# Kernel tuning notes

Hardware: AMD Instinct MI355X
Metric: run time of the kernel (lower is better)

## Reference

```python
import jax, jax.numpy as jnp
import numpy as np

GROUP_MANTISSA = 8
GROUP_SIZE = 36


def bfp_quantize(x, mantissa=GROUP_MANTISSA, group_size=GROUP_SIZE):
    """Block floating point: flatten, group consecutive group_size elements,
    share the max exponent within each group, keep `mantissa` mantissa bits."""
    flat = x.reshape(-1)
    n = flat.shape[0]
    pad = (-n) % group_size
    f = jnp.pad(flat, (0, pad)).reshape(-1, group_size)  # [G, group_size]
    m = jnp.max(jnp.abs(f), axis=1, keepdims=True)       # group max magnitude
    safe_m = jnp.where(m > 0, m, jnp.ones_like(m))
    e = jnp.floor(jnp.log2(safe_m))                      # shared exponent
    scale = jnp.exp2(e - (mantissa - 1))                 # LSB step for the group
    q = jnp.round(f / scale) * scale
    q = jnp.where(m > 0, q, jnp.zeros_like(q))
    return q.reshape(-1)[:n].reshape(x.shape)


def setup_inputs() -> dict:
    key = jax.random.key(0)
    kx, kw, kb = jax.random.split(key, 3)
    x = jax.random.normal(kx, (32, 64, 112, 112), dtype=jnp.float32)
    # kaiming-uniform-ish scale for a 3x3x64 fan-in
    fan_in = 64 * 3 * 3
    bound = 1.0 / np.sqrt(fan_in)
    weight = jax.random.uniform(kw, (64, 64, 3, 3), dtype=jnp.float32, minval=-bound, maxval=bound) * np.sqrt(3.0)
    bias = jax.random.uniform(kb, (64,), dtype=jnp.float32, minval=-bound, maxval=bound)
    return {"x": x, "weight": weight, "bias": bias}


def reference(x, weight, bias):
    xq = bfp_quantize(x)
    wq = bfp_quantize(weight)
    out = jax.lax.conv_general_dilated(
        xq, wq,
        window_strides=(1, 1),
        padding=((1, 1), (1, 1)),
        lhs_dilation=(1, 1),
        rhs_dilation=(1, 1),
        dimension_numbers=("NCHW", "OIHW", "NCHW"),
        feature_group_count=1,
    )
    return out + bias[None, :, None, None]
```

## Files before the change

kernel.cpp:

```cpp
#include <hip/hip_runtime.h>
#include <hip/hip_bf16.h>

typedef __attribute__((ext_vector_type(4))) float f32x4;
typedef __attribute__((ext_vector_type(8))) short s16x8;

#define X_ELEMS 25690112
#define X_F4    6422528
#define NG_FULL 713614
#define NG      713615
#define HW 112
#define CHW (64*112*112)

__device__ __forceinline__ unsigned short f32_to_bf16_exact(float q) {
    return (unsigned short)(__float_as_uint(q) >> 16);
}

__device__ __forceinline__ void scale_from_max(float m, float& scale, float& inv) {
    if (m > 0.f) {
        int e = (int)((__float_as_uint(m) >> 23) & 0xFF) - 127;
        scale = __builtin_ldexpf(1.0f, e - 7);
        inv   = __builtin_ldexpf(1.0f, 7 - e);
    } else { scale = 0.f; inv = 0.f; }
}

__global__ __launch_bounds__(256) void q1_scales(const float* __restrict__ x,
                                                 float2* __restrict__ sc) {
    __shared__ float lmax[2304];
    int b = blockIdx.x, tid = threadIdx.x;
    long base4 = (long)b * 2304;
    #pragma unroll
    for (int it = 0; it < 9; ++it) {
        int i = it * 256 + tid;
        long g4 = base4 + i;
        float m = 0.f;
        if (g4 < X_F4) {
            float4 v = ((const float4*)x)[g4];
            m = fmaxf(fmaxf(fabsf(v.x), fabsf(v.y)), fmaxf(fabsf(v.z), fabsf(v.w)));
        }
        lmax[i] = m;
    }
    __syncthreads();
    int g = b * 256 + tid;
    if (g < NG) {
        float m = 0.f;
        int o = tid * 9;
        #pragma unroll
        for (int j = 0; j < 9; ++j) m = fmaxf(m, lmax[o + j]);
        float s, inv; scale_from_max(m, s, inv);
        sc[g] = make_float2(s, inv);
    }
}

__global__ __launch_bounds__(256) void qw_kernel(const float* __restrict__ w,
                                                 unsigned short* __restrict__ wt) {
    int g = blockIdx.x * 256 + threadIdx.x;
    if (g >= 1024) return;
    const float4* p = (const float4*)w + g * 9;
    float vv[36]; float m = 0.f;
    #pragma unroll
    for (int i = 0; i < 9; ++i) {
        float4 v = p[i];
        vv[i*4+0]=v.x; vv[i*4+1]=v.y; vv[i*4+2]=v.z; vv[i*4+3]=v.w;
        m = fmaxf(m, fmaxf(fmaxf(fabsf(v.x), fabsf(v.y)), fmaxf(fabsf(v.z), fabsf(v.w))));
    }
    float s, inv; scale_from_max(m, s, inv);
    #pragma unroll
    for (int j = 0; j < 36; ++j) {
        int flat = g * 36 + j;
        int k = flat / 576, rem = flat % 576;
        int c = rem / 9, pp = rem % 9;
        float q = rintf(vv[j] * inv) * s;
        wt[pp * 4096 + k * 64 + c] = f32_to_bf16_exact(q);
    }
}

__global__ __launch_bounds__(256) void q2_quant(const float* __restrict__ x,
                                               const float2* __restrict__ sc,
                                               unsigned short* __restrict__ xt) {
    int n = blockIdx.y, h = blockIdx.x;
    int tid = threadIdx.x;
    int cg = tid >> 7;
    int wv = tid & 127;
    if (wv >= HW) return;
    int base = n * CHW + h * HW + wv;
    int ob = ((n * HW + h) * HW + wv) * 64 + cg * 32;
    #pragma unroll
    for (int jo = 0; jo < 4; ++jo) {
        union { unsigned short u[8]; uint4 d; } pk;
        #pragma unroll
        for (int j = 0; j < 8; ++j) {
            int c = cg * 32 + jo * 8 + j;
            unsigned off = (unsigned)(base + c * 12544);
            float v = x[off];
            float2 s = sc[off / 36u];
            pk.u[j] = f32_to_bf16_exact(rintf(v * s.y) * s.x);
        }
        *(uint4*)(xt + ob + jo * 8) = pk.d;
    }
}

__global__ __launch_bounds__(256, 2) void conv_mfma(const unsigned short* __restrict__ xt,
                                                    const unsigned short* __restrict__ wt,
                                                    const float* __restrict__ bias,
                                                    float* __restrict__ out) {
    __shared__ unsigned short xs[300 * 72];
    const int tid = threadIdx.x;
    const int wave = tid >> 6, lane = tid & 63;
    const int wl = lane & 15, quad = lane >> 4;
    const int kg = wave & 1, mg = wave >> 1;
    const int b = blockIdx.x;
    const int n = b / 56, rem = b % 56;
    const int h0 = (rem >> 2) * 8, w0 = (rem & 3) * 28;

    #pragma unroll
    for (int it = 0; it < 10; ++it) {
        int q = it * 256 + tid;
        if (q < 2400) {
            int pixel = q >> 3, sub = q & 7;
            int r = pixel / 30, col = pixel % 30;
            int hh = h0 + r - 1, ww = w0 + col - 1;
            uint4 v = {0u, 0u, 0u, 0u};
            if (hh >= 0 && hh < HW && ww >= 0 && ww < HW)
                v = *(const uint4*)(xt + (((n * HW + hh) * HW + ww) << 6) + sub * 8);
            *(uint4*)&xs[pixel * 72 + sub * 8] = v;
        }
    }

    s16x8 Bf[9][2][2];
    #pragma unroll
    for (int p = 0; p < 9; ++p)
        #pragma unroll
        for (int cs = 0; cs < 2; ++cs)
            #pragma unroll
            for (int j = 0; j < 2; ++j)
                Bf[p][cs][j] = *(const s16x8*)(wt + p * 4096 +
                                ((kg * 2 + j) * 16 + wl) * 64 + cs * 32 + quad * 8);

    float bv[2];
    #pragma unroll
    for (int j = 0; j < 2; ++j) bv[j] = bias[kg * 32 + j * 16 + wl];

    int pixb[7], eofs[7];
    #pragma unroll
    for (int mti = 0; mti < 7; ++mti) {
        int m = (mg * 7 + mti) * 16 + wl;
        pixb[mti] = (m / 28) * 30 + (m % 28);
        int m0 = (mg * 7 + mti) * 16 + quad * 4;
        eofs[mti] = (m0 / 28) * HW + (m0 % 28);
    }

    __syncthreads();

    f32x4 acc[7][2];
    f32x4 zero = {0.f, 0.f, 0.f, 0.f};
    #pragma unroll
    for (int mti = 0; mti < 7; ++mti) { acc[mti][0] = zero; acc[mti][1] = zero; }

    #pragma unroll
    for (int p = 0; p < 9; ++p) {
        const int dpix = (p / 3) * 30 + (p % 3);
        #pragma unroll
        for (int cs = 0; cs < 2; ++cs) {
            const int cofs = cs * 32 + quad * 8;
            #pragma unroll
            for (int mti = 0; mti < 7; ++mti) {
                s16x8 A = *(const s16x8*)&xs[(pixb[mti] + dpix) * 72 + cofs];
                acc[mti][0] = __builtin_amdgcn_mfma_f32_16x16x32_bf16(A, Bf[p][cs][0], acc[mti][0], 0, 0, 0);
                acc[mti][1] = __builtin_amdgcn_mfma_f32_16x16x32_bf16(A, Bf[p][cs][1], acc[mti][1], 0, 0, 0);
            }
        }
    }

    int obase = n * CHW + h0 * HW + w0;
    #pragma unroll
    for (int mti = 0; mti < 7; ++mti) {
        #pragma unroll
        for (int j = 0; j < 2; ++j) {
            f32x4 v = acc[mti][j];
            v.x += bv[j]; v.y += bv[j]; v.z += bv[j]; v.w += bv[j];
            *(f32x4*)(out + obase + (kg * 32 + j * 16 + wl) * 12544 + eofs[mti]) = v;
        }
    }
}

extern "C" void kernel_launch(void* const* d_in, const int* in_sizes, int n_in,
                              void* d_out, int out_size, void* d_ws, size_t ws_size,
                              hipStream_t stream) {
    const float* x    = (const float*)d_in[0];
    const float* w    = (const float*)d_in[1];
    const float* bias = (const float*)d_in[2];
    float* out = (float*)d_out;
    char* ws = (char*)d_ws;
    unsigned short* xt = (unsigned short*)ws;
    unsigned short* wt = (unsigned short*)(ws + 51380224);
    float2*         sc = (float2*)(ws + 51380224 + 73728);

    hipLaunchKernelGGL(q1_scales, dim3(2788),    dim3(256), 0, stream, x, sc);
    hipLaunchKernelGGL(qw_kernel, dim3(4),       dim3(256), 0, stream, w, wt);
    hipLaunchKernelGGL(q2_quant,  dim3(112, 32), dim3(256), 0, stream, x, sc, xt);
    hipLaunchKernelGGL(conv_mfma, dim3(1792),    dim3(256), 0, stream, xt, wt, bias, out);
}
```

Measured before the change: 302.5 us.

## Persistent double-buffered conv with async LDS loads and channel-octet padded layout

Weight quantization moves into an extra block of the scale kernel, which also zeroes a pad buffer, so one launch disappears. The quantized activations are stored in a channel-octet layout with padded rows, and the quant kernel becomes fully coalesced per pixel. The conv kernel becomes persistent with 256 blocks looping over 7 tiles. Each tile is prefetched into a double-buffered LDS with global_load_lds and an XOR swizzle to hide load latency and avoid bank conflicts. Weights are now reloaded from global or cache inside the loop instead of held in registers, which adds memory traffic in exchange for lower register pressure.

```diff
diff --git a/kernel.cpp b/kernel.cpp
--- a/kernel.cpp
+++ b/kernel.cpp
@@ -1,20 +1,28 @@
 #include <hip/hip_runtime.h>
-#include <hip/hip_bf16.h>
 
 typedef __attribute__((ext_vector_type(4))) float f32x4;
 typedef __attribute__((ext_vector_type(8))) short s16x8;
-
-#define X_ELEMS 25690112
-#define X_F4    6422528
-#define NG_FULL 713614
-#define NG      713615
+typedef __attribute__((ext_vector_type(4))) unsigned int u32x4;
+
 #define HW 112
+#define PW8 116
+#define ROWS8 (PW8*8)
+#define PLANE8 (112*ROWS8)
 #define CHW (64*112*112)
+#define NG 713615
+#define X_F4 6422528
+
+#define XQ8_BYTES 53215232
+#define WT_OFF    53219328
+#define SC_OFF    53293056
+#define ZP_OFF    59001984
 
 __device__ __forceinline__ unsigned short f32_to_bf16_exact(float q) {
     return (unsigned short)(__float_as_uint(q) >> 16);
 }
-
+__device__ __forceinline__ unsigned int pack_bf16x2(float a, float b) {
+    return __builtin_amdgcn_perm(__float_as_uint(b), __float_as_uint(a), 0x07060302u);
+}
 __device__ __forceinline__ void scale_from_max(float m, float& scale, float& inv) {
     if (m > 0.f) {
         int e = (int)((__float_as_uint(m) >> 23) & 0xFF) - 127;
@@ -24,9 +32,39 @@
 }
 
 __global__ __launch_bounds__(256) void q1_scales(const float* __restrict__ x,
-                                                 float2* __restrict__ sc) {
+                                                 const float* __restrict__ w,
+                                                 float2* __restrict__ sc,
+                                                 unsigned short* __restrict__ wt,
+                                                 u32x4* __restrict__ zp) {
     __shared__ float lmax[2304];
-    int b = blockIdx.x, tid = threadIdx.x;
+    const int b = blockIdx.x, tid = threadIdx.x;
+
+    if (b == 2788) {
+        if (tid < 64) zp[tid] = (u32x4){0u, 0u, 0u, 0u};
+        #pragma unroll 1
+        for (int rep = 0; rep < 4; ++rep) {
+            int g = rep * 256 + tid;
+            const float4* p = (const float4*)w + g * 9;
+            float vv[36]; float m = 0.f;
+            #pragma unroll
+            for (int i = 0; i < 9; ++i) {
+                float4 v = p[i];
+                vv[i*4+0]=v.x; vv[i*4+1]=v.y; vv[i*4+2]=v.z; vv[i*4+3]=v.w;
+                m = fmaxf(m, fmaxf(fmaxf(fabsf(v.x), fabsf(v.y)), fmaxf(fabsf(v.z), fabsf(v.w))));
+            }
+            float s, inv; scale_from_max(m, s, inv);
+            #pragma unroll
+            for (int j = 0; j < 36; ++j) {
+                int flat = g * 36 + j;
+                int k = flat / 576, rem = flat % 576;
+                int c = rem / 9, pp = rem % 9;
+                float q = rintf(vv[j] * inv) * s;
+                wt[pp * 4096 + k * 64 + c] = f32_to_bf16_exact(q);
+            }
+        }
+        return;
+    }
+
     long base4 = (long)b * 2304;
     #pragma unroll
     for (int it = 0; it < 9; ++it) {
@@ -42,8 +80,7 @@
     __syncthreads();
     int g = b * 256 + tid;
     if (g < NG) {
-        float m = 0.f;
-        int o = tid * 9;
+        float m = 0.f; int o = tid * 9;
         #pragma unroll
         for (int j = 0; j < 9; ++j) m = fmaxf(m, lmax[o + j]);
         float s, inv; scale_from_max(m, s, inv);
@@ -51,134 +88,138 @@
     }
 }
 
-__global__ __launch_bounds__(256) void qw_kernel(const float* __restrict__ w,
-                                                 unsigned short* __restrict__ wt) {
-    int g = blockIdx.x * 256 + threadIdx.x;
-    if (g >= 1024) return;
-    const float4* p = (const float4*)w + g * 9;
-    float vv[36]; float m = 0.f;
-    #pragma unroll
-    for (int i = 0; i < 9; ++i) {
-        float4 v = p[i];
-        vv[i*4+0]=v.x; vv[i*4+1]=v.y; vv[i*4+2]=v.z; vv[i*4+3]=v.w;
-        m = fmaxf(m, fmaxf(fmaxf(fabsf(v.x), fabsf(v.y)), fmaxf(fabsf(v.z), fabsf(v.w))));
-    }
-    float s, inv; scale_from_max(m, s, inv);
-    #pragma unroll
-    for (int j = 0; j < 36; ++j) {
-        int flat = g * 36 + j;
-        int k = flat / 576, rem = flat % 576;
-        int c = rem / 9, pp = rem % 9;
-        float q = rintf(vv[j] * inv) * s;
-        wt[pp * 4096 + k * 64 + c] = f32_to_bf16_exact(q);
-    }
-}
-
 __global__ __launch_bounds__(256) void q2_quant(const float* __restrict__ x,
-                                               const float2* __restrict__ sc,
-                                               unsigned short* __restrict__ xt) {
-    int n = blockIdx.y, h = blockIdx.x;
-    int tid = threadIdx.x;
-    int cg = tid >> 7;
-    int wv = tid & 127;
-    if (wv >= HW) return;
-    int base = n * CHW + h * HW + wv;
-    int ob = ((n * HW + h) * HW + wv) * 64 + cg * 32;
-    #pragma unroll
-    for (int jo = 0; jo < 4; ++jo) {
-        union { unsigned short u[8]; uint4 d; } pk;
-        #pragma unroll
-        for (int j = 0; j < 8; ++j) {
-            int c = cg * 32 + jo * 8 + j;
-            unsigned off = (unsigned)(base + c * 12544);
-            float v = x[off];
-            float2 s = sc[off / 36u];
-            pk.u[j] = f32_to_bf16_exact(rintf(v * s.y) * s.x);
-        }
-        *(uint4*)(xt + ob + jo * 8) = pk.d;
-    }
-}
-
-__global__ __launch_bounds__(256, 2) void conv_mfma(const unsigned short* __restrict__ xt,
-                                                    const unsigned short* __restrict__ wt,
-                                                    const float* __restrict__ bias,
-                                                    float* __restrict__ out) {
-    __shared__ unsigned short xs[300 * 72];
+                                                const float2* __restrict__ sc,
+                                                unsigned short* __restrict__ xq8) {
+    int blk = blockIdx.x;
+    int pb = blk % 49; int t2 = blk / 49; int oct = t2 & 7; int n = t2 >> 3;
+    int p = pb * 256 + threadIdx.x;
+    int h = p / 112, ww = p - h * 112;
+    unsigned short* row = xq8 + ((n * 8 + oct) * 112 + h) * ROWS8;
+    int cbase = (n * 64 + oct * 8) * 12544 + p;
+    unsigned int pk[4];
+    #pragma unroll
+    for (int jj = 0; jj < 4; ++jj) {
+        int f0 = cbase + (2 * jj) * 12544;
+        int f1 = f0 + 12544;
+        float2 s0 = sc[(unsigned)f0 / 36u];
+        float2 s1 = sc[(unsigned)f1 / 36u];
+        float q0 = rintf(x[f0] * s0.y) * s0.x;
+        float q1 = rintf(x[f1] * s1.y) * s1.x;
+        pk[jj] = pack_bf16x2(q0, q1);
+    }
+    *(u32x4*)(row + (ww + 2) * 8) = (u32x4){pk[0], pk[1], pk[2], pk[3]};
+    u32x4 z4 = {0u, 0u, 0u, 0u};
+    if (ww == 0)        { *(u32x4*)(row) = z4;            *(u32x4*)(row + 8) = z4; }
+    else if (ww == 111) { *(u32x4*)(row + 114 * 8) = z4;  *(u32x4*)(row + 115 * 8) = z4; }
+}
+
+__global__ __launch_bounds__(256) void conv_mfma(const unsigned short* __restrict__ xq8,
+                                                 const unsigned short* __restrict__ wt,
+                                                 const float* __restrict__ bias,
+                                                 float* __restrict__ out,
+                                                 const unsigned short* __restrict__ zp) {
+    __shared__ unsigned short xs[2][3328 * 8];
     const int tid = threadIdx.x;
     const int wave = tid >> 6, lane = tid & 63;
     const int wl = lane & 15, quad = lane >> 4;
     const int kg = wave & 1, mg = wave >> 1;
-    const int b = blockIdx.x;
-    const int n = b / 56, rem = b % 56;
-    const int h0 = (rem >> 2) * 8, w0 = (rem & 3) * 28;
-
-    #pragma unroll
-    for (int it = 0; it < 10; ++it) {
-        int q = it * 256 + tid;
-        if (q < 2400) {
-            int pixel = q >> 3, sub = q & 7;
-            int r = pixel / 30, col = pixel % 30;
-            int hh = h0 + r - 1, ww = w0 + col - 1;
-            uint4 v = {0u, 0u, 0u, 0u};
-            if (hh >= 0 && hh < HW && ww >= 0 && ww < HW)
-                v = *(const uint4*)(xt + (((n * HW + hh) * HW + ww) << 6) + sub * 8);
-            *(uint4*)&xs[pixel * 72 + sub * 8] = v;
-        }
-    }
-
-    s16x8 Bf[9][2][2];
-    #pragma unroll
-    for (int p = 0; p < 9; ++p)
-        #pragma unroll
-        for (int cs = 0; cs < 2; ++cs)
-            #pragma unroll
-            for (int j = 0; j < 2; ++j)
-                Bf[p][cs][j] = *(const s16x8*)(wt + p * 4096 +
-                                ((kg * 2 + j) * 16 + wl) * 64 + cs * 32 + quad * 8);
+    const int bs = blockIdx.x;
+
+    unsigned pk13[13];
+    #pragma unroll
+    for (int k = 0; k < 13; ++k) {
+        int g = (wave * 13 + k) * 64 + lane;
+        if (g < 3200) {
+            int oct = g / 400, rem = g - oct * 400;
+            int r = rem / 40, pix = rem - r * 40;
+            int pixs = pix ^ oct;
+            pk13[k] = ((unsigned)r << 24) | (unsigned)(oct * PLANE8 + pixs * 8);
+        } else pk13[k] = 0xFF000000u;
+    }
 
     float bv[2];
     #pragma unroll
     for (int j = 0; j < 2; ++j) bv[j] = bias[kg * 32 + j * 16 + wl];
-
-    int pixb[7], eofs[7];
+    int pixb[7];
     #pragma unroll
     for (int mti = 0; mti < 7; ++mti) {
         int m = (mg * 7 + mti) * 16 + wl;
-        pixb[mti] = (m / 28) * 30 + (m % 28);
-        int m0 = (mg * 7 + mti) * 16 + quad * 4;
-        eofs[mti] = (m0 / 28) * HW + (m0 % 28);
-    }
-
-    __syncthreads();
-
-    f32x4 acc[7][2];
-    f32x4 zero = {0.f, 0.f, 0.f, 0.f};
-    #pragma unroll
-    for (int mti = 0; mti < 7; ++mti) { acc[mti][0] = zero; acc[mti][1] = zero; }
-
-    #pragma unroll
-    for (int p = 0; p < 9; ++p) {
-        const int dpix = (p / 3) * 30 + (p % 3);
-        #pragma unroll
-        for (int cs = 0; cs < 2; ++cs) {
-            const int cofs = cs * 32 + quad * 8;
-            #pragma unroll
-            for (int mti = 0; mti < 7; ++mti) {
-                s16x8 A = *(const s16x8*)&xs[(pixb[mti] + dpix) * 72 + cofs];
-                acc[mti][0] = __builtin_amdgcn_mfma_f32_16x16x32_bf16(A, Bf[p][cs][0], acc[mti][0], 0, 0, 0);
-                acc[mti][1] = __builtin_amdgcn_mfma_f32_16x16x32_bf16(A, Bf[p][cs][1], acc[mti][1], 0, 0, 0);
-            }
-        }
-    }
-
-    int obase = n * CHW + h0 * HW + w0;
-    #pragma unroll
-    for (int mti = 0; mti < 7; ++mti) {
-        #pragma unroll
-        for (int j = 0; j < 2; ++j) {
-            f32x4 v = acc[mti][j];
-            v.x += bv[j]; v.y += bv[j]; v.z += bv[j]; v.w += bv[j];
-            *(f32x4*)(out + obase + (kg * 32 + j * 16 + wl) * 12544 + eofs[mti]) = v;
+        pixb[mti] = (m / 28) * 40 + (m % 28) + 1;
+    }
+
+    auto issue = [&](int ti, int bi) {
+        int t = bs + 256 * ti;
+        int st = ((t & 7) * 224) + (t >> 3);
+        int n = st / 56, rem = st - n * 56;
+        int h0 = (rem >> 2) * 8, w0 = (rem & 3) * 28;
+        const unsigned short* base = xq8 + n * 8 * PLANE8 + w0 * 8;
+        #pragma unroll
+        for (int k = 0; k < 13; ++k) {
+            unsigned pk = pk13[k];
+            int r = (int)(pk >> 24);
+            int hh = h0 - 1 + r;
+            bool ok = (r <= 9) && (hh >= 0) && (hh < HW);
+            const unsigned short* src = ok ? (base + (pk & 0xFFFFFFu) + hh * ROWS8) : zp;
+            unsigned short* dst = (unsigned short*)&xs[bi][(wave * 13 + k) * 512];
+            __builtin_amdgcn_global_load_lds(
+                (const __attribute__((address_space(1))) void*)src,
+                (__attribute__((address_space(3))) void*)dst, 16, 0, 0);
+        }
+    };
+
+    issue(0, 0);
+
+    #pragma unroll 1
+    for (int i = 0; i < 7; ++i) {
+        asm volatile("s_waitcnt vmcnt(0)" ::: "memory");
+        __builtin_amdgcn_s_barrier();
+        if (i < 6) issue(i + 1, (i + 1) & 1);
+
+        int t = bs + 256 * i;
+        int st = ((t & 7) * 224) + (t >> 3);
+        int n = st / 56, rem = st - n * 56;
+        int h0 = (rem >> 2) * 8, w0 = (rem & 3) * 28;
+        const unsigned short* xb = &xs[i & 1][0];
+
+        f32x4 acc[7][2];
+        f32x4 zero = {0.f, 0.f, 0.f, 0.f};
+        #pragma unroll
+        for (int mti = 0; mti < 7; ++mti) { acc[mti][0] = zero; acc[mti][1] = zero; }
+
+        #pragma unroll
+        for (int p = 0; p < 9; ++p) {
+            const int dpix = (p / 3) * 40 + (p % 3);
+            #pragma unroll
+            for (int cs = 0; cs < 2; ++cs) {
+                const int oq = cs * 4 + quad;
+                s16x8 B0 = *(const s16x8*)(wt + p * 4096 + ((kg * 2 + 0) * 16 + wl) * 64 + cs * 32 + quad * 8);
+                s16x8 B1 = *(const s16x8*)(wt + p * 4096 + ((kg * 2 + 1) * 16 + wl) * 64 + cs * 32 + quad * 8);
+                s16x8 A[7];
+                #pragma unroll
+                for (int mti = 0; mti < 7; ++mti) {
+                    int pix = pixb[mti] + dpix;
+                    A[mti] = *(const s16x8*)(xb + (oq * 400 + (pix ^ oq)) * 8);
+                }
+                #pragma unroll
+                for (int mti = 0; mti < 7; ++mti) {
+                    acc[mti][0] = __builtin_amdgcn_mfma_f32_16x16x32_bf16(A[mti], B0, acc[mti][0], 0, 0, 0);
+                    acc[mti][1] = __builtin_amdgcn_mfma_f32_16x16x32_bf16(A[mti], B1, acc[mti][1], 0, 0, 0);
+                }
+            }
+        }
+
+        int obase = n * CHW + h0 * HW + w0;
+        #pragma unroll
+        for (int mti = 0; mti < 7; ++mti) {
+            int m0 = (mg * 7 + mti) * 16 + quad * 4;
+            int eofs = (m0 / 28) * HW + (m0 % 28);
+            #pragma unroll
+            for (int j = 0; j < 2; ++j) {
+                f32x4 v = acc[mti][j];
+                v.x += bv[j]; v.y += bv[j]; v.z += bv[j]; v.w += bv[j];
+                *(f32x4*)(out + obase + (kg * 32 + j * 16 + wl) * 12544 + eofs) = v;
+            }
         }
     }
 }
@@ -191,12 +232,12 @@
     const float* bias = (const float*)d_in[2];
     float* out = (float*)d_out;
     char* ws = (char*)d_ws;
-    unsigned short* xt = (unsigned short*)ws;
-    unsigned short* wt = (unsigned short*)(ws + 51380224);
-    float2*         sc = (float2*)(ws + 51380224 + 73728);
-
-    hipLaunchKernelGGL(q1_scales, dim3(2788),    dim3(256), 0, stream, x, sc);
-    hipLaunchKernelGGL(qw_kernel, dim3(4),       dim3(256), 0, stream, w, wt);
-    hipLaunchKernelGGL(q2_quant,  dim3(112, 32), dim3(256), 0, stream, x, sc, xt);
-    hipLaunchKernelGGL(conv_mfma, dim3(1792),    dim3(256), 0, stream, xt, wt, bias, out);
-}
+    unsigned short* xq8 = (unsigned short*)ws;
+    unsigned short* wt  = (unsigned short*)(ws + WT_OFF);
+    float2*         sc  = (float2*)(ws + SC_OFF);
+    unsigned short* zp  = (unsigned short*)(ws + ZP_OFF);
+
+    hipLaunchKernelGGL(q1_scales, dim3(2789),  dim3(256), 0, stream, x, w, sc, wt, (u32x4*)zp);
+    hipLaunchKernelGGL(q2_quant,  dim3(12544), dim3(256), 0, stream, x, sc, xq8);
+    hipLaunchKernelGGL(conv_mfma, dim3(256),   dim3(256), 0, stream, xq8, wt, bias, out, zp);
+}
```

Result: faster. 273.1 us (-9.7%).
